# Performance work log

Hardware: AMD Instinct MI355X
Metric: run time of the kernel (lower is better)

The kernel has to match this reference:

```python
import jax, jax.numpy as jnp
import numpy as np

DIM = 100      # number of assets in the basket
M = 50         # time steps
T = 1.0
R = 0.05
SIGMA = 0.2
S0 = 100.0
DT = T / M
H = 128        # hidden_dim of ZetaNetwork
B = 8192       # Monte-Carlo paths (batch)
EPS = 1e-5     # torch LayerNorm eps


def _layernorm(x, g, b):
    mu = jnp.mean(x, axis=-1, keepdims=True)
    var = jnp.mean((x - mu) ** 2, axis=-1, keepdims=True)
    return (x - mu) / jnp.sqrt(var + EPS) * g + b


def setup_inputs() -> dict:
    key = jax.random.key(0)
    ks = jax.random.split(key, 12)
    dw = jax.random.normal(ks[0], (B, M, DIM), dtype=jnp.float32)
    t_grid = jax.random.uniform(ks[1], (B, M), dtype=jnp.float32)
    s = 0.05
    inp = {
        "dw": dw,
        "t_grid": t_grid,
        "W1": jax.random.normal(ks[2], (DIM + 1, H), dtype=jnp.float32) * s,
        "b1": jnp.zeros((H,), jnp.float32),
        "g1": jnp.ones((H,), jnp.float32),
        "be1": jnp.zeros((H,), jnp.float32),
        "W2": jax.random.normal(ks[3], (H, H), dtype=jnp.float32) * s,
        "b2": jnp.zeros((H,), jnp.float32),
        "g2": jnp.ones((H,), jnp.float32),
        "be2": jnp.zeros((H,), jnp.float32),
        "W3": jax.random.normal(ks[4], (H, H), dtype=jnp.float32) * s,
        "b3": jnp.zeros((H,), jnp.float32),
        "g3": jnp.ones((H,), jnp.float32),
        "be3": jnp.zeros((H,), jnp.float32),
        "W4": jax.random.normal(ks[5], (H, DIM), dtype=jnp.float32) * s,
        "b4": jnp.zeros((DIM,), jnp.float32),
        "Y0": jnp.array([10.0], dtype=jnp.float32),
    }
    return inp


def reference(dw, t_grid, W1, b1, g1, be1, W2, b2, g2, be2,
              W3, b3, g3, be3, W4, b4, Y0):
    batch = dw.shape[0]

    def zeta_net(x):  # x: [B, DIM+1]
        h = jax.nn.gelu(_layernorm(x @ W1 + b1, g1, be1), approximate=False)
        h = jax.nn.gelu(_layernorm(h @ W2 + b2, g2, be2), approximate=False)
        h = jax.nn.gelu(_layernorm(h @ W3 + b3, g3, be3), approximate=False)
        return jax.nn.sigmoid(h @ W4 + b4)  # [B, DIM]

    def step(carry, xs):
        S, Y = carry
        dw_i, t_i = xs                                   # [B,DIM], [B,1]
        net_in = jnp.concatenate([S / S0, t_i], axis=1)  # [B,DIM+1]
        zeta = zeta_net(net_in)
        dS = S * (R * DT + SIGMA * dw_i)
        portfolio_gain = jnp.sum(zeta * dS, axis=1, keepdims=True)
        asset_val = jnp.sum(zeta * S, axis=1, keepdims=True)
        Y = Y + R * (Y - asset_val) * DT + portfolio_gain
        S = S + dS
        return (S, Y), None

    S_init = jnp.full((batch, DIM), S0, dtype=dw.dtype)
    Y_init = jnp.ones((batch, 1), dtype=dw.dtype) * Y0
    xs = (jnp.swapaxes(dw, 0, 1),                # [M,B,DIM]
          jnp.swapaxes(t_grid, 0, 1)[..., None])  # [M,B,1]
    (S, Y), _ = jax.lax.scan(step, (S_init, Y_init), xs)
    return (Y, S)
```

## Files before the change

### kernel.cpp

```cpp
#include <hip/hip_runtime.h>
#include <hip/hip_bf16.h>
#include <cstdint>
#include <cstddef>

typedef __attribute__((ext_vector_type(8))) short short8;
typedef __attribute__((ext_vector_type(4))) float f32x4;
typedef __attribute__((ext_vector_type(2))) float f32x2;
typedef __attribute__((ext_vector_type(4))) unsigned int u32x4;

#define NDIM 100
#define NSTEP 50
#define NPATH 8192
#define XSTR 128
#define ESTR 128

typedef const __attribute__((address_space(1))) unsigned int glb_u32;
typedef __attribute__((address_space(3))) unsigned int lds_u32;

__device__ __forceinline__ unsigned short f2b(float f){
  unsigned int u = __float_as_uint(f);
  u += 0x7fffu + ((u >> 16) & 1u);
  return (unsigned short)(u >> 16);
}
__device__ __forceinline__ float b2f(unsigned short h){
  return __uint_as_float(((unsigned int)h) << 16);
}

template<int CTRL>
__device__ __forceinline__ float dpp_add(float x){
  int t = __builtin_amdgcn_update_dpp(0, __float_as_int(x), CTRL, 0xF, 0xF, true);
  return x + __int_as_float(t);
}
__device__ __forceinline__ float rowsum16(float x){
  x = dpp_add<0x128>(x);
  x = dpp_add<0x124>(x);
  x = dpp_add<0x122>(x);
  x = dpp_add<0x121>(x);
  return x;
}

__global__ __launch_bounds__(256) void prep_all(
    const float* __restrict__ W1, const float* __restrict__ W2,
    const float* __restrict__ W3, const float* __restrict__ W4,
    const float* __restrict__ b1, const float* __restrict__ g1, const float* __restrict__ be1,
    const float* __restrict__ b2, const float* __restrict__ g2, const float* __restrict__ be2,
    const float* __restrict__ b3, const float* __restrict__ g3, const float* __restrict__ be3,
    const float* __restrict__ b4,
    unsigned short* __restrict__ WTS, float* __restrict__ PPAR)
{
  if (blockIdx.x < 256){
    int idx = blockIdx.x * 256 + threadIdx.x;
    int j = idx & 7;
    int s = (idx >> 3) & 15;
    int n = (idx >> 7) & 127;
    int L = idx >> 14;
    int lc = s ^ (n & 15);
    int k  = j * 16 + lc;
    float v;
    if (L == 0)      v = (k <= NDIM) ? W1[k * 128 + n] : 0.f;
    else if (L == 1) v = W2[k * 128 + n];
    else if (L == 2) v = W3[k * 128 + n];
    else             v = (n < NDIM) ? W4[k * NDIM + n] : 0.f;
    WTS[idx] = f2b(v);
    return;
  }
  int idx = (blockIdx.x - 256) * 256 + threadIdx.x;
  if (idx >= 1536) return;
  int ct = idx & 7;
  int c  = (idx >> 3) & 15;
  int p  = (idx >> 7) % 3;
  int L  = idx / 384;
  int col = ct * 16 + c;
  const float* v;
  if (L == 0)      v = (p == 0) ? b1 : (p == 1) ? g1 : be1;
  else if (L == 1) v = (p == 0) ? b2 : (p == 1) ? g2 : be2;
  else if (L == 2) v = (p == 0) ? b3 : (p == 1) ? g3 : be3;
  else             v = b4;
  float val;
  if (L == 3) val = (p == 0 && col < NDIM) ? b4[col] : 0.f;
  else        val = v[col];
  PPAR[idx] = val;
}

__global__ __launch_bounds__(256) void phaseA(
    const float* __restrict__ dw, const float* __restrict__ tg,
    unsigned short* __restrict__ X, unsigned short* __restrict__ E,
    float* __restrict__ Sout, int path0)
{
  const int pb = threadIdx.x >> 6;
  const int t  = threadIdx.x & 63;
  const int bl = blockIdx.x * 4 + pb;
  const int b  = path0 + bl;
  const int d0 = (t & 7) * 16 + (t >> 3);
  const int d1 = d0 + 8;
  float s0 = 100.f, s1 = 100.f;
  const float* dwb = dw + (long)b * NSTEP * NDIM;
  const float* tgb = tg + (long)b * NSTEP;
  unsigned short* Xb = X + (long)bl * NSTEP * XSTR;
  unsigned short* Eb = E + (long)bl * NSTEP * ESTR;
  for (int i = 0; i < NSTEP; ++i){
    float tv = tgb[i];
    float w0 = (d0 < NDIM) ? dwb[i * NDIM + d0] : 0.f;
    float w1 = (d1 < NDIM) ? dwb[i * NDIM + d1] : 0.f;
    unsigned short* Xr = Xb + i * XSTR;
    unsigned short* Er = Eb + i * ESTR;
    if (d0 < NDIM)       Xr[t] = f2b(s0 * 0.01f);
    else if (d0 == NDIM) Xr[t] = f2b(tv);
    if (d1 < NDIM)       Xr[t + 64] = f2b(s1 * 0.01f);
    Er[t]      = (d0 < NDIM) ? f2b(0.2f * s0 * w0) : (unsigned short)0;
    Er[t + 64] = (d1 < NDIM) ? f2b(0.2f * s1 * w1) : (unsigned short)0;
    s0 = fmaf(s0, 0.001f + 0.2f * w0, s0);
    s1 = fmaf(s1, 0.001f + 0.2f * w1, s1);
  }
  if (d0 < NDIM) Sout[(long)b * NDIM + d0] = s0;
  if (d1 < NDIM) Sout[(long)b * NDIM + d1] = s1;
}

__global__ __launch_bounds__(256, 3) void phaseB(
    const unsigned short* __restrict__ X,
    const unsigned short* __restrict__ E,
    const unsigned short* __restrict__ WTS,
    const float* __restrict__ PPAR,
    float* __restrict__ cbuf, long row0)
{
  __shared__ __align__(16) char lds[49152];
  char* const wbuf = lds;
  const int tid = threadIdx.x;
  const int w = tid >> 6;
  const int l = tid & 63;
  const int g = l >> 4;
  const int c = l & 15;
  char* const H = lds + 32768 + w * 4096;
  const long base = (long)blockIdx.x * 128 + w * 16;

  auto stage = [&](int Loff){
    #pragma unroll
    for (int it = 0; it < 8; ++it){
      int chunk = w * 8 + it;
      __builtin_amdgcn_global_load_lds((glb_u32*)(WTS + Loff + chunk * 512 + l * 8),
          (lds_u32*)(wbuf + chunk * 1024), 16, 0, 0);
    }
  };

  short8 af0[4], af1[4];
  {
    const unsigned short* xr0 = X + (base + c) * XSTR;
    const unsigned short* xr1 = X + (base + 64 + c) * XSTR;
    #pragma unroll
    for (int ks = 0; ks < 4; ++ks){
      af0[ks] = *(const short8*)(xr0 + 32 * ks + 8 * g);
      af1[ks] = *(const short8*)(xr1 + 32 * ks + 8 * g);
    }
  }

  auto mfma2 = [&](f32x4 (&acc0)[8], f32x4 (&acc1)[8], f32x4 blo, f32x4 bhi){
    #pragma unroll
    for (int ct = 0; ct < 8; ++ct){
      float bs = (ct < 4) ? blo[ct] : bhi[ct - 4];
      f32x4 z; z[0] = bs; z[1] = bs; z[2] = bs; z[3] = bs;
      acc0[ct] = z; acc1[ct] = z;
      const char* rowp = wbuf + ((ct * 16 + c) << 8);
      #pragma unroll
      for (int ks = 0; ks < 4; ++ks){
        short8 bf = *(const short8*)(rowp + (((4 * ks + g) ^ c) << 4));
        acc0[ct] = __builtin_amdgcn_mfma_f32_16x16x32_bf16(af0[ks], bf, acc0[ct], 0, 0, 0);
        acc1[ct] = __builtin_amdgcn_mfma_f32_16x16x32_bf16(af1[ks], bf, acc1[ct], 0, 0, 0);
      }
    }
  };

  auto gelu2 = [&](f32x2 y) -> f32x2 {
    f32x2 a = y * -2.4554673f;
    f32x2 u;
    u[0] = __builtin_amdgcn_exp2f(a[0]);
    u[1] = __builtin_amdgcn_exp2f(a[1]);
    f32x2 d = u + 1.0f;
    f32x2 r;
    r[0] = __builtin_amdgcn_rcpf(d[0]);
    r[1] = __builtin_amdgcn_rcpf(d[1]);
    return y * r;
  };

  auto postproc = [&](f32x4 (&acc)[8], short8 (&af)[4],
                      f32x4 glo, f32x4 ghi, f32x4 belo, f32x4 behi){
    f32x2 sA = {0.f, 0.f}, sB = {0.f, 0.f}, qA = {0.f, 0.f}, qB = {0.f, 0.f};
    #pragma unroll
    for (int ct = 0; ct < 8; ++ct){
      f32x2 xy = __builtin_shufflevector(acc[ct], acc[ct], 0, 1);
      f32x2 zw = __builtin_shufflevector(acc[ct], acc[ct], 2, 3);
      sA += xy; qA += xy * xy;
      sB += zw; qB += zw * zw;
    }
    sA[0] = rowsum16(sA[0]); sA[1] = rowsum16(sA[1]);
    sB[0] = rowsum16(sB[0]); sB[1] = rowsum16(sB[1]);
    qA[0] = rowsum16(qA[0]); qA[1] = rowsum16(qA[1]);
    qB[0] = rowsum16(qB[0]); qB[1] = rowsum16(qB[1]);
    f32x2 muA = sA * 0.0078125f, muB = sB * 0.0078125f;
    f32x2 vA = qA * 0.0078125f - muA * muA + 1e-5f;
    f32x2 vB = qB * 0.0078125f - muB * muB + 1e-5f;
    f32x2 rA, rB;
    rA[0] = rsqrtf(vA[0]); rA[1] = rsqrtf(vA[1]);
    rB[0] = rsqrtf(vB[0]); rB[1] = rsqrtf(vB[1]);
    u32x4 ov0, ov1, ov2, ov3;
    #pragma unroll
    for (int p = 0; p < 4; ++p){
      float ga0 = (p < 2) ? glo[2*p]     : ghi[2*p - 4];
      float ga1 = (p < 2) ? glo[2*p + 1] : ghi[2*p - 3];
      float be0 = (p < 2) ? belo[2*p]     : behi[2*p - 4];
      float be1 = (p < 2) ? belo[2*p + 1] : behi[2*p - 3];
      f32x2 xyE = __builtin_shufflevector(acc[2*p],   acc[2*p],   0, 1);
      f32x2 zwE = __builtin_shufflevector(acc[2*p],   acc[2*p],   2, 3);
      f32x2 xyO = __builtin_shufflevector(acc[2*p+1], acc[2*p+1], 0, 1);
      f32x2 zwO = __builtin_shufflevector(acc[2*p+1], acc[2*p+1], 2, 3);
      f32x2 AEA = rA * ga0, AEB = rB * ga0;
      f32x2 AOA = rA * ga1, AOB = rB * ga1;
      f32x2 hEA = gelu2(xyE * AEA + (be0 - muA * AEA));
      f32x2 hEB = gelu2(zwE * AEB + (be0 - muB * AEB));
      f32x2 hOA = gelu2(xyO * AOA + (be1 - muA * AOA));
      f32x2 hOB = gelu2(zwO * AOB + (be1 - muB * AOB));
      unsigned int k0, k1, k2, k3;
      asm("v_cvt_pk_bf16_f32 %0, %1, %2" : "=v"(k0) : "v"(hEA[0]), "v"(hOA[0]));
      asm("v_cvt_pk_bf16_f32 %0, %1, %2" : "=v"(k1) : "v"(hEA[1]), "v"(hOA[1]));
      asm("v_cvt_pk_bf16_f32 %0, %1, %2" : "=v"(k2) : "v"(hEB[0]), "v"(hOB[0]));
      asm("v_cvt_pk_bf16_f32 %0, %1, %2" : "=v"(k3) : "v"(hEB[1]), "v"(hOB[1]));
      ov0[p] = k0; ov1[p] = k1; ov2[p] = k2; ov3[p] = k3;
    }
    int r0 = 4 * g;
    *(u32x4*)(H + (r0 + 0) * 256 + ((c ^ (r0 + 0)) << 4)) = ov0;
    *(u32x4*)(H + (r0 + 1) * 256 + ((c ^ (r0 + 1)) << 4)) = ov1;
    *(u32x4*)(H + (r0 + 2) * 256 + ((c ^ (r0 + 2)) << 4)) = ov2;
    *(u32x4*)(H + (r0 + 3) * 256 + ((c ^ (r0 + 3)) << 4)) = ov3;
    #pragma unroll
    for (int ks = 0; ks < 4; ++ks)
      af[ks] = *(const short8*)(H + c * 256 + (((4 * ks + g) ^ c) << 4));
  };

  auto epilogue = [&](f32x4 (&acc)[8], short8 (&ep)[4], long rbase){
    f32x2 pgA = {0.f, 0.f}, pgB = {0.f, 0.f};
    #pragma unroll
    for (int ct = 0; ct < 8; ++ct){
      f32x2 xy = __builtin_shufflevector(acc[ct], acc[ct], 0, 1);
      f32x2 zw = __builtin_shufflevector(acc[ct], acc[ct], 2, 3);
      f32x2 aA = xy * -1.4426950f, aB = zw * -1.4426950f;
      f32x2 u, d, r;
      u[0] = __builtin_amdgcn_exp2f(aA[0]); u[1] = __builtin_amdgcn_exp2f(aA[1]);
      d = u + 1.f;
      r[0] = __builtin_amdgcn_rcpf(d[0]); r[1] = __builtin_amdgcn_rcpf(d[1]);
      f32x2 eA = { b2f((unsigned short)ep[0][ct]), b2f((unsigned short)ep[1][ct]) };
      pgA += r * eA;
      u[0] = __builtin_amdgcn_exp2f(aB[0]); u[1] = __builtin_amdgcn_exp2f(aB[1]);
      d = u + 1.f;
      r[0] = __builtin_amdgcn_rcpf(d[0]); r[1] = __builtin_amdgcn_rcpf(d[1]);
      f32x2 eB = { b2f((unsigned short)ep[2][ct]), b2f((unsigned short)ep[3][ct]) };
      pgB += r * eB;
    }
    pgA[0] = rowsum16(pgA[0]); pgA[1] = rowsum16(pgA[1]);
    pgB[0] = rowsum16(pgB[0]); pgB[1] = rowsum16(pgB[1]);
    if (c == 0){
      cbuf[row0 + rbase + 4 * g + 0] = pgA[0];
      cbuf[row0 + rbase + 4 * g + 1] = pgA[1];
      cbuf[row0 + rbase + 4 * g + 2] = pgB[0];
      cbuf[row0 + rbase + 4 * g + 3] = pgB[1];
    }
  };

  stage(0);
  __syncthreads();

  #pragma unroll
  for (int L = 0; L < 3; ++L){
    const float* pp = PPAR + L * 384 + c * 8;
    f32x4 blo  = *(const f32x4*)pp,         bhi  = *(const f32x4*)(pp + 4);
    f32x4 acc0[8], acc1[8];
    mfma2(acc0, acc1, blo, bhi);
    f32x4 glo  = *(const f32x4*)(pp + 128), ghi  = *(const f32x4*)(pp + 132);
    f32x4 belo = *(const f32x4*)(pp + 256), behi = *(const f32x4*)(pp + 260);
    __syncthreads();
    stage((L + 1) * 16384);
    postproc(acc0, af0, glo, ghi, belo, behi);
    postproc(acc1, af1, glo, ghi, belo, behi);
    __syncthreads();
  }

  {
    const float* pp = PPAR + 3 * 384 + c * 8;
    f32x4 blo = *(const f32x4*)pp, bhi = *(const f32x4*)(pp + 4);
    short8 ep0[4], ep1[4];
    #pragma unroll
    for (int j = 0; j < 4; ++j){
      ep0[j] = *(const short8*)(E + (base + 4 * g + j) * ESTR + c * 8);
      ep1[j] = *(const short8*)(E + (base + 64 + 4 * g + j) * ESTR + c * 8);
    }
    f32x4 acc0[8], acc1[8];
    mfma2(acc0, acc1, blo, bhi);
    epilogue(acc0, ep0, base);
    epilogue(acc1, ep1, base + 64);
  }
}

__global__ __launch_bounds__(256) void phaseC(const float* __restrict__ cbuf,
                                              const float* __restrict__ Y0,
                                              float* __restrict__ Yout)
{
  int b = blockIdx.x * 256 + threadIdx.x;
  if (b >= NPATH) return;
  const float kk = 1.0f + 0.05f * (1.0f / 50.0f);
  float y = Y0[0];
  const float* cb = cbuf + (long)b * NSTEP;
  #pragma unroll 10
  for (int i = 0; i < NSTEP; ++i) y = y * kk + cb[i];
  Yout[b] = y;
}

extern "C" void kernel_launch(void* const* d_in, const int* in_sizes, int n_in,
                              void* d_out, int out_size, void* d_ws, size_t ws_size,
                              hipStream_t stream)
{
  const float* dw  = (const float*)d_in[0];
  const float* tg  = (const float*)d_in[1];
  const float* W1  = (const float*)d_in[2];
  const float* b1  = (const float*)d_in[3];
  const float* g1  = (const float*)d_in[4];
  const float* be1 = (const float*)d_in[5];
  const float* W2  = (const float*)d_in[6];
  const float* b2  = (const float*)d_in[7];
  const float* g2  = (const float*)d_in[8];
  const float* be2 = (const float*)d_in[9];
  const float* W3  = (const float*)d_in[10];
  const float* b3  = (const float*)d_in[11];
  const float* g3  = (const float*)d_in[12];
  const float* be3 = (const float*)d_in[13];
  const float* W4  = (const float*)d_in[14];
  const float* b4  = (const float*)d_in[15];
  const float* Y0  = (const float*)d_in[16];
  float* out = (float*)d_out;

  char* ws = (char*)d_ws;
  unsigned short* WTS = (unsigned short*)ws;
  float* PPAR = (float*)(ws + 131072);
  float* cbuf = (float*)(ws + 137344);
  char* chunk = ws + 1775744;

  prep_all<<<262, 256, 0, stream>>>(W1, W2, W3, W4,
      b1, g1, be1, b2, g2, be2, b3, g3, be3, b4, WTS, PPAR);

  long avail = (long)ws_size - 1775744L;
  long pc = (avail > 0) ? (avail / 25600L) : 0;
  if (pc > 8192) pc = 8192;
  pc -= pc % 128;
  if (pc < 128) pc = 128;

  for (long p0 = 0; p0 < 8192; p0 += pc){
    long np = 8192 - p0; if (np > pc) np = pc;
    unsigned short* Xc = (unsigned short*)chunk;
    unsigned short* Ec = Xc + np * 50L * XSTR;
    phaseA<<<(int)(np / 4), 256, 0, stream>>>(dw, tg, Xc, Ec, out + 8192, (int)p0);
    long nrows = np * 50L;
    phaseB<<<(int)(nrows / 128), 256, 0, stream>>>(Xc, Ec, WTS, PPAR, cbuf, p0 * 50L);
  }
  phaseC<<<32, 256, 0, stream>>>(cbuf, Y0, out);
}
```

Before: 237.1 us.

## Recompute portfolio increment in phaseB from X and dw instead of storing E

```diff
diff --git a/kernel.cpp b/kernel.cpp
--- a/kernel.cpp
+++ b/kernel.cpp
@@ -12,7 +12,6 @@
 #define NSTEP 50
 #define NPATH 8192
 #define XSTR 128
-#define ESTR 128
 
 typedef const __attribute__((address_space(1))) unsigned int glb_u32;
 typedef __attribute__((address_space(3))) unsigned int lds_u32;
@@ -84,7 +83,7 @@
 
 __global__ __launch_bounds__(256) void phaseA(
     const float* __restrict__ dw, const float* __restrict__ tg,
-    unsigned short* __restrict__ X, unsigned short* __restrict__ E,
+    unsigned short* __restrict__ X,
     float* __restrict__ Sout, int path0)
 {
   const int pb = threadIdx.x >> 6;
@@ -97,18 +96,13 @@
   const float* dwb = dw + (long)b * NSTEP * NDIM;
   const float* tgb = tg + (long)b * NSTEP;
   unsigned short* Xb = X + (long)bl * NSTEP * XSTR;
-  unsigned short* Eb = E + (long)bl * NSTEP * ESTR;
   for (int i = 0; i < NSTEP; ++i){
     float tv = tgb[i];
     float w0 = (d0 < NDIM) ? dwb[i * NDIM + d0] : 0.f;
     float w1 = (d1 < NDIM) ? dwb[i * NDIM + d1] : 0.f;
     unsigned short* Xr = Xb + i * XSTR;
-    unsigned short* Er = Eb + i * ESTR;
-    if (d0 < NDIM)       Xr[t] = f2b(s0 * 0.01f);
-    else if (d0 == NDIM) Xr[t] = f2b(tv);
-    if (d1 < NDIM)       Xr[t + 64] = f2b(s1 * 0.01f);
-    Er[t]      = (d0 < NDIM) ? f2b(0.2f * s0 * w0) : (unsigned short)0;
-    Er[t + 64] = (d1 < NDIM) ? f2b(0.2f * s1 * w1) : (unsigned short)0;
+    Xr[t]      = (d0 < NDIM) ? f2b(s0 * 0.01f) : ((d0 == NDIM) ? f2b(tv) : (unsigned short)0);
+    Xr[t + 64] = (d1 < NDIM) ? f2b(s1 * 0.01f) : (unsigned short)0;
     s0 = fmaf(s0, 0.001f + 0.2f * w0, s0);
     s1 = fmaf(s1, 0.001f + 0.2f * w1, s1);
   }
@@ -118,10 +112,10 @@
 
 __global__ __launch_bounds__(256, 3) void phaseB(
     const unsigned short* __restrict__ X,
-    const unsigned short* __restrict__ E,
+    const float* __restrict__ dw,
     const unsigned short* __restrict__ WTS,
     const float* __restrict__ PPAR,
-    float* __restrict__ cbuf, long row0)
+    float* __restrict__ cbuf, long row0, int p0)
 {
   __shared__ __align__(16) char lds[49152];
   char* const wbuf = lds;
@@ -235,6 +229,23 @@
       af[ks] = *(const short8*)(H + c * 256 + (((4 * ks + g) ^ c) << 4));
   };
 
+  auto load_e = [&](long rl) -> short8 {
+    int rli = (int)rl;
+    int pl = rli / 50;
+    int st = rli - pl * 50;
+    const float* dwr = dw + ((long)(p0 + pl) * 50 + st) * 100;
+    short8 x8 = *(const short8*)(X + rl * XSTR + c * 8);
+    short8 ev;
+    #pragma unroll
+    for (int ct = 0; ct < 8; ++ct){
+      int n = ct * 16 + c;
+      float wv = (n < NDIM) ? dwr[n] : 0.f;
+      float e = 20.f * b2f((unsigned short)x8[ct]) * wv;
+      ev[ct] = (short)f2b(e);
+    }
+    return ev;
+  };
+
   auto epilogue = [&](f32x4 (&acc)[8], short8 (&ep)[4], long rbase){
     f32x2 pgA = {0.f, 0.f}, pgB = {0.f, 0.f};
     #pragma unroll
@@ -288,8 +299,8 @@
     short8 ep0[4], ep1[4];
     #pragma unroll
     for (int j = 0; j < 4; ++j){
-      ep0[j] = *(const short8*)(E + (base + 4 * g + j) * ESTR + c * 8);
-      ep1[j] = *(const short8*)(E + (base + 64 + 4 * g + j) * ESTR + c * 8);
+      ep0[j] = load_e(base + 4 * g + j);
+      ep1[j] = load_e(base + 64 + 4 * g + j);
     }
     f32x4 acc0[8], acc1[8];
     mfma2(acc0, acc1, blo, bhi);
@@ -345,18 +356,18 @@
       b1, g1, be1, b2, g2, be2, b3, g3, be3, b4, WTS, PPAR);
 
   long avail = (long)ws_size - 1775744L;
-  long pc = (avail > 0) ? (avail / 25600L) : 0;
-  if (pc > 8192) pc = 8192;
+  long pc = (avail > 0) ? (avail / 12800L) : 0;
+  if (pc > 4096) pc = 4096;
   pc -= pc % 128;
   if (pc < 128) pc = 128;
 
   for (long p0 = 0; p0 < 8192; p0 += pc){
     long np = 8192 - p0; if (np > pc) np = pc;
     unsigned short* Xc = (unsigned short*)chunk;
-    unsigned short* Ec = Xc + np * 50L * XSTR;
-    phaseA<<<(int)(np / 4), 256, 0, stream>>>(dw, tg, Xc, Ec, out + 8192, (int)p0);
+    phaseA<<<(int)(np / 4), 256, 0, stream>>>(dw, tg, Xc, out + 8192, (int)p0);
     long nrows = np * 50L;
-    phaseB<<<(int)(nrows / 128), 256, 0, stream>>>(Xc, Ec, WTS, PPAR, cbuf, p0 * 50L);
+    phaseB<<<(int)(nrows / 128), 256, 0, stream>>>(Xc, dw, WTS, PPAR, cbuf,
+        p0 * 50L, (int)p0);
   }
   phaseC<<<32, 256, 0, stream>>>(cbuf, Y0, out);
 }
```

Result: slower. 256.3 us (+8.1%).
